# Performance work log

Measured on AMD Instinct MI355X. Metric: run time of the kernel, lower is better.

## Reference

```python
import jax, jax.numpy as jnp
import numpy as np

N, E, B = 50000, 800000, 1000
NODE_DIN, BB_DOUT, DHID, K = 32, 64, 64, 3
GLOB_DIN, EMBED_DIN = 64, 64
CIN = BB_DOUT + NODE_DIN  # 96


def setup_inputs() -> dict:
    key = jax.random.key(0)
    ks = jax.random.split(key, 24)

    def w(k, shape, fan_in):
        return jax.random.normal(k, shape, jnp.float32) / np.float32(np.sqrt(fan_in))

    inp = dict(
        x=jax.random.normal(ks[0], (N, NODE_DIN), jnp.float32),
        u=jax.random.normal(ks[1], (B, GLOB_DIN), jnp.float32),
        z=jax.random.normal(ks[2], (N, BB_DOUT), jnp.float32),
        edge_index=jax.random.randint(ks[3], (2, E), 0, N),
        edge_weight=jax.random.uniform(ks[4], (E,), jnp.float32),
        batch=jnp.sort(jax.random.randint(ks[5], (N,), 0, B)),
        batch_size=B,
        prev_h=jax.random.normal(ks[6], (N, DHID), jnp.float32),
    )
    # six ChebConvs of GConvGRU: x-convs take CIN, h-convs take DHID; all output DHID
    for i, nm in enumerate(["xz", "hz", "xr", "hr", "xh", "hh"]):
        cin = CIN if nm[0] == "x" else DHID
        inp[f"W{nm}"] = w(ks[7 + 2 * i], (K, cin, DHID), cin * K)
        inp[f"b{nm}"] = jnp.zeros((DHID,), jnp.float32)
    inp["Wg"] = w(ks[20], (GLOB_DIN, EMBED_DIN), GLOB_DIN)
    inp["bg"] = jnp.zeros((EMBED_DIN,), jnp.float32)
    return inp


def _cheb(xin, W, b, src, dst, w_norm, n):
    """ChebConv with sym norm, lambda_max=2 -> L_hat = -D^-1/2 A D^-1/2 (diag cancels)."""
    def prop(t):  # L_hat @ t  ([N,C])
        return -jax.ops.segment_sum(w_norm[:, None] * t[src], dst, num_segments=n)

    out = xin @ W[0] + b
    tx_prev = xin
    tx = None
    if W.shape[0] > 1:
        tx = prop(xin)
        out = out + tx @ W[1]
    for k in range(2, W.shape[0]):
        tx_new = 2.0 * prop(tx) - tx_prev
        out = out + tx_new @ W[k]
        tx_prev, tx = tx, tx_new
    return out


def reference(x, u, z, edge_index, edge_weight, batch, batch_size, prev_h,
              Wxz, bxz, Whz, bhz, Wxr, bxr, Whr, bhr, Wxh, bxh, Whh, bhh, Wg, bg):
    n = x.shape[0]
    src, dst = edge_index[0], edge_index[1]
    deg = jax.ops.segment_sum(edge_weight, src, num_segments=n)
    deg_safe = jnp.where(deg > 0, deg, 1.0)
    dinv = jnp.where(deg > 0, jax.lax.rsqrt(deg_safe), 0.0)
    w_norm = dinv[src] * edge_weight * dinv[dst]

    xin = jnp.concatenate([z, x], axis=-1)  # [N, CIN]
    Z = jax.nn.sigmoid(_cheb(xin, Wxz, bxz, src, dst, w_norm, n)
                       + _cheb(prev_h, Whz, bhz, src, dst, w_norm, n))
    R = jax.nn.sigmoid(_cheb(xin, Wxr, bxr, src, dst, w_norm, n)
                       + _cheb(prev_h, Whr, bhr, src, dst, w_norm, n))
    Ht = jnp.tanh(_cheb(xin, Wxh, bxh, src, dst, w_norm, n)
                  + _cheb(prev_h * R, Whh, bhh, src, dst, w_norm, n))
    h = Z * prev_h + (1.0 - Z) * Ht

    graph_emb = jax.ops.segment_sum(z, batch, num_segments=batch_size)  # [B, BB_DOUT]
    global_emb = jax.nn.relu(u @ Wg + bg)                                # [B, EMBED_DIN]
    fused = jnp.concatenate([graph_emb, global_emb], axis=-1)           # [B, 128]
    return fused, h
```

## Files before the change

kernel.cpp:

```cpp
#include <hip/hip_runtime.h>

#define NN 50000
#define EE 800000
#define BB 1000
#define NB 196
#define NR 8
#define RS 6272
#define NC 32
#define CHUNK 25000

#define NRB 160
#define RSB 314
#define NBIN 256
#define CH2 3125
#define CAP 7000

typedef unsigned short u16;
typedef unsigned long long u64;
typedef __attribute__((ext_vector_type(8))) short bf16x8;
typedef __attribute__((ext_vector_type(4))) float f32x4;

static __device__ __forceinline__ u16 f2b(float f) {
    union { float f; unsigned u; } v;
    v.f = f;
    unsigned r = v.u + 0x7fffu + ((v.u >> 16) & 1u);
    return (u16)(r >> 16);
}

static __device__ __forceinline__ float b2f(short s) {
    union { unsigned u; float f; } c;
    c.u = ((unsigned)(u16)s) << 16;
    return c.f;
}

__global__ __launch_bounds__(512) void k_degcnt_lds(
    const int* __restrict__ src, const int* __restrict__ dst,
    const float* __restrict__ ew, float* __restrict__ deg_p,
    int* __restrict__ cnt_p) {
    __shared__ float sdeg[RS];
    __shared__ int scnt[RS];
    int r = blockIdx.x & (NR - 1);
    int c = blockIdx.x >> 3;
    int base = r * RS;
    for (int i = threadIdx.x; i < RS; i += 512) {
        sdeg[i] = 0.f;
        scnt[i] = 0;
    }
    __syncthreads();
    int e0 = c * CHUNK;
    for (int j = threadIdx.x; j < CHUNK; j += 512) {
        int e = e0 + j;
        int s = src[e], d = dst[e];
        int sl = s - base, dl = d - base;
        if ((unsigned)sl < RS) atomicAdd(&sdeg[sl], ew[e]);
        if ((unsigned)dl < RS) atomicAdd(&scnt[dl], 1);
    }
    __syncthreads();
    int lim = (NN - base < RS) ? (NN - base) : RS;
    for (int i = threadIdx.x; i < lim; i += 512) {
        deg_p[(size_t)c * NN + base + i] = sdeg[i];
        cnt_p[(size_t)c * NN + base + i] = scnt[i];
    }
}

__global__ void k_scan1(const int* __restrict__ cnt_p, int* __restrict__ cnt,
                        int* __restrict__ incl, int* __restrict__ bsum) {
    __shared__ int s[256];
    int i = blockIdx.x * 256 + threadIdx.x;
    int v = 0;
    if (i < NN) {
#pragma unroll
        for (int p = 0; p < NC; p++) v += cnt_p[(size_t)p * NN + i];
        cnt[i] = v;
    }
    s[threadIdx.x] = v;
    __syncthreads();
    for (int off = 1; off < 256; off <<= 1) {
        int t = (threadIdx.x >= off) ? s[threadIdx.x - off] : 0;
        __syncthreads();
        s[threadIdx.x] += t;
        __syncthreads();
    }
    if (i < NN) incl[i] = s[threadIdx.x];
    if (threadIdx.x == 255) bsum[blockIdx.x] = s[255];
}

__global__ void k_scan2(int* __restrict__ bsum) {
    __shared__ int s[256];
    int v = (threadIdx.x < NB) ? bsum[threadIdx.x] : 0;
    s[threadIdx.x] = v;
    __syncthreads();
    for (int off = 1; off < 256; off <<= 1) {
        int t = (threadIdx.x >= off) ? s[threadIdx.x - off] : 0;
        __syncthreads();
        s[threadIdx.x] += t;
        __syncthreads();
    }
    if (threadIdx.x < NB) bsum[threadIdx.x] = s[threadIdx.x];
}

__global__ void k_scan3(const int* __restrict__ incl, const int* __restrict__ cnt,
                        const int* __restrict__ bsum, int* __restrict__ row_ptr,
                        int* __restrict__ scur, const float* __restrict__ deg_p,
                        float* __restrict__ dinv) {
    int i = blockIdx.x * 256 + threadIdx.x;
    if (i >= NN) return;
    int off = (blockIdx.x > 0) ? bsum[blockIdx.x - 1] : 0;
    int start = off + incl[i] - cnt[i];
    row_ptr[i] = start;
    if (i % RSB == 0) scur[i / RSB] = start;
    float d = 0.f;
#pragma unroll
    for (int p = 0; p < NC; p++) d += deg_p[(size_t)p * NN + i];
    dinv[i] = d > 0.f ? rsqrtf(d) : 0.f;
}

__global__ __launch_bounds__(512) void k_bin(
    const int* __restrict__ src, const int* __restrict__ dst,
    const float* __restrict__ ew, const float* __restrict__ dinv,
    int* __restrict__ scur, u64* __restrict__ stage) {
    __shared__ int cntA[NRB], baseB[NRB], rk[NRB];
    int e0 = blockIdx.x * CH2;
    for (int i = threadIdx.x; i < NRB; i += 512) cntA[i] = 0;
    __syncthreads();
    for (int j = threadIdx.x; j < CH2; j += 512) {
        int d = dst[e0 + j];
        atomicAdd(&cntA[d / RSB], 1);
    }
    __syncthreads();
    for (int i = threadIdx.x; i < NRB; i += 512) {
        baseB[i] = atomicAdd(&scur[i], cntA[i]);
        rk[i] = 0;
    }
    __syncthreads();
    for (int j = threadIdx.x; j < CH2; j += 512) {
        int e = e0 + j;
        int d = dst[e], s = src[e];
        int r = d / RSB;
        int slot = baseB[r] + atomicAdd(&rk[r], 1);
        float w = dinv[s] * ew[e] * dinv[d];
        unsigned dl = (unsigned)(d - r * RSB);
        u64 rec = ((u64)((dl << 16) | (unsigned)s) << 32) | (u64)__float_as_uint(w);
        stage[slot] = rec;
    }
}

__global__ __launch_bounds__(512) void k_sortrange(
    const u64* __restrict__ stage, const int* __restrict__ row_ptr,
    uint2* __restrict__ csr8) {
    __shared__ uint2 img[CAP];
    __shared__ int cur[RSB];
    int r = blockIdx.x;
    int r0 = r * RSB;
    int nrows = (NN - r0 < RSB) ? (NN - r0) : RSB;
    int p0 = row_ptr[r0];
    int p1 = (r0 + nrows < NN) ? row_ptr[r0 + nrows] : EE;
    for (int i = threadIdx.x; i < nrows; i += 512) cur[i] = row_ptr[r0 + i] - p0;
    __syncthreads();
    int n = p1 - p0;
    for (int j = threadIdx.x; j < n; j += 512) {
        u64 rec = stage[p0 + j];
        unsigned hi = (unsigned)(rec >> 32);
        int pos = atomicAdd(&cur[hi >> 16], 1);
        img[pos] = make_uint2(hi & 0xffffu, (unsigned)(rec & 0xffffffffu));
    }
    __syncthreads();
    for (int j = threadIdx.x; j < n; j += 512) csr8[p0 + j] = img[j];
}

__global__ void k_build_A(const float* __restrict__ z, const float* __restrict__ x,
                          const float* __restrict__ ph, u16* __restrict__ A) {
    int i = blockIdx.x * 256 + threadIdx.x;
    if (i >= NN * 160) return;
    int n = i / 160, c = i - n * 160;
    float v;
    if (c < 64) v = z[n * 64 + c];
    else if (c < 96) v = x[n * 32 + (c - 64)];
    else v = ph[n * 64 + (c - 96)];
    A[(size_t)n * 480 + c] = f2b(v);
}

__global__ void k_packW_all(const float* __restrict__ Wxz, const float* __restrict__ Wxr,
                            const float* __restrict__ Wxh, const float* __restrict__ Whz,
                            const float* __restrict__ Whr, const float* __restrict__ Whh,
                            u16* __restrict__ Wp, u16* __restrict__ W3p) {
    int idx = blockIdx.x * 256 + threadIdx.x;
    if (idx < 15 * 12 * 512) {
        int j = idx & 7, l = (idx >> 3) & 63;
        int ct = (idx >> 9) % 12, s = (idx >> 9) / 12;
        int k = 32 * s + (l >> 4) * 8 + j;
        int g = ct >> 2;
        int c = 16 * (ct & 3) + (l & 15);
        bool isX;
        int kr;
        if (k < 96)       { isX = true;  kr = k; }
        else if (k < 160) { isX = false; kr = k - 96; }
        else if (k < 256) { isX = true;  kr = 96 + (k - 160); }
        else if (k < 320) { isX = false; kr = 64 + (k - 256); }
        else if (k < 416) { isX = true;  kr = 192 + (k - 320); }
        else              { isX = false; kr = 128 + (k - 416); }
        float val;
        if (isX) {
            const float* W = (g == 0) ? Wxz : ((g == 1) ? Wxr : Wxh);
            val = W[kr * 64 + c];
        } else if (g == 2) {
            val = 0.f;
        } else {
            const float* W = (g == 0) ? Whz : Whr;
            val = W[kr * 64 + c];
        }
        Wp[idx] = f2b(val);
    } else {
        int i2 = idx - 15 * 12 * 512;
        if (i2 >= 6 * 4 * 512) return;
        int j = i2 & 7, l = (i2 >> 3) & 63;
        int ct = (i2 >> 9) & 3, s = i2 >> 11;
        int k = 32 * s + (l >> 4) * 8 + j;
        int ki = k >> 6, kr = k & 63;
        int c = 16 * ct + (l & 15);
        W3p[i2] = f2b(Whh[(ki * 64 + kr) * 64 + c]);
    }
}

template <int C, int SCALE, bool HB, int BS, int OS>
__global__ __launch_bounds__(BS) void k_pull(
    const u16* __restrict__ Abase, int inofs, int baseofs, int outofs,
    const uint2* __restrict__ csr8, const int* __restrict__ row_ptr,
    const int* __restrict__ cnt) {
    constexpr int TPR = C / 8;
    int tid = blockIdx.x * BS + threadIdx.x;
    int r = tid / TPR;
    int c8 = (tid - r * TPR) * 8;
    if (r >= NN) return;
    int s0 = row_ptr[r], n = cnt[r];
    float acc[8] = {0.f, 0.f, 0.f, 0.f, 0.f, 0.f, 0.f, 0.f};
    const u16* in = Abase + inofs + c8;
    uint2 e = (n > 0) ? csr8[s0] : make_uint2(0u, 0u);
    for (int j = 0; j < n; j++) {
        uint2 ec = e;
        if (j + 1 < n) e = csr8[s0 + j + 1];
        float w = __uint_as_float(ec.y);
        bf16x8 v = *(const bf16x8*)(in + (size_t)ec.x * OS);
#pragma unroll
        for (int k = 0; k < 8; k++) acc[k] += w * b2f(v[k]);
    }
    const float sc = -(float)SCALE;
    float o[8];
    if (HB) {
        bf16x8 b = *(const bf16x8*)(Abase + (size_t)r * OS + baseofs + c8);
#pragma unroll
        for (int k = 0; k < 8; k++) o[k] = sc * acc[k] - b2f(b[k]);
    } else {
#pragma unroll
        for (int k = 0; k < 8; k++) o[k] = sc * acc[k];
    }
    bf16x8 p;
#pragma unroll
    for (int k = 0; k < 8; k++) p[k] = (short)f2b(o[k]);
    *(bf16x8*)(const_cast<u16*>(Abase) + (size_t)r * OS + outofs + c8) = p;
}

__global__ __launch_bounds__(256) void k_gates_mfma(
    const u16* __restrict__ A, const u16* __restrict__ Wp,
    const float* __restrict__ bxz, const float* __restrict__ bhz,
    const float* __restrict__ bxr, const float* __restrict__ bhr,
    const float* __restrict__ bxh,
    u16* __restrict__ Zb16, u16* __restrict__ Hx16, u16* __restrict__ A3) {
    int gw = (blockIdx.x * 256 + threadIdx.x) >> 6;
    int tile = gw / 3;
    int g = gw - tile * 3;
    int r0 = tile * 16;
    if (r0 >= NN) return;
    int lane = threadIdx.x & 63;
    int q = lane >> 4, j0 = lane & 15;

    f32x4 acc[4];
#pragma unroll
    for (int i = 0; i < 4; i++) acc[i] = (f32x4){0.f, 0.f, 0.f, 0.f};

    const u16* arow = A + (size_t)(r0 + j0) * 480 + q * 8;
    if (g < 2) {
        const u16* bp0 = Wp + (size_t)(g * 4) * 512 + lane * 8;
#pragma unroll
        for (int s = 0; s < 15; s++) {
            bf16x8 a = *(const bf16x8*)(arow + 32 * s);
            const u16* bp = bp0 + (size_t)(s * 12) * 512;
#pragma unroll
            for (int ct = 0; ct < 4; ct++) {
                bf16x8 b = *(const bf16x8*)(bp + ct * 512);
                acc[ct] = __builtin_amdgcn_mfma_f32_16x16x32_bf16(a, b, acc[ct], 0, 0, 0);
            }
        }
    } else {
        const int slist[9] = {0, 1, 2, 5, 6, 7, 10, 11, 12};
        const u16* bp0 = Wp + (size_t)8 * 512 + lane * 8;
#pragma unroll
        for (int si = 0; si < 9; si++) {
            int s = slist[si];
            bf16x8 a = *(const bf16x8*)(arow + 32 * s);
            const u16* bp = bp0 + (size_t)(s * 12) * 512;
#pragma unroll
            for (int ct = 0; ct < 4; ct++) {
                bf16x8 b = *(const bf16x8*)(bp + ct * 512);
                acc[ct] = __builtin_amdgcn_mfma_f32_16x16x32_bf16(a, b, acc[ct], 0, 0, 0);
            }
        }
    }

    if (g == 0) {
#pragma unroll
        for (int ct = 0; ct < 4; ct++) {
            int j = 16 * ct + j0;
            float bz = bxz[j] + bhz[j];
#pragma unroll
            for (int reg = 0; reg < 4; reg++) {
                int r = r0 + q * 4 + reg;
                float zv = 1.f / (1.f + expf(-(acc[ct][reg] + bz)));
                Zb16[(size_t)r * 64 + j] = f2b(zv);
            }
        }
    } else if (g == 1) {
#pragma unroll
        for (int ct = 0; ct < 4; ct++) {
            int j = 16 * ct + j0;
            float br = bxr[j] + bhr[j];
#pragma unroll
            for (int reg = 0; reg < 4; reg++) {
                int r = r0 + q * 4 + reg;
                float rv = 1.f / (1.f + expf(-(acc[ct][reg] + br)));
                float phv = b2f((short)A[(size_t)r * 480 + 96 + j]);
                A3[(size_t)r * 192 + j] = f2b(rv * phv);
            }
        }
    } else {
#pragma unroll
        for (int ct = 0; ct < 4; ct++) {
            int j = 16 * ct + j0;
            float bh = bxh[j];
#pragma unroll
            for (int reg = 0; reg < 4; reg++) {
                int r = r0 + q * 4 + reg;
                Hx16[(size_t)r * 64 + j] = f2b(acc[ct][reg] + bh);
            }
        }
    }
}

__global__ __launch_bounds__(256) void k_final_mfma(
    const u16* __restrict__ A3, const u16* __restrict__ W3p,
    const float* __restrict__ bhh, const u16* __restrict__ Hx16,
    const u16* __restrict__ Zb16, const u16* __restrict__ A,
    float* __restrict__ outh) {
    int wv = (blockIdx.x * 256 + threadIdx.x) >> 6;
    int lane = threadIdx.x & 63;
    int r0 = wv * 16;
    if (r0 >= NN) return;
    int q = lane >> 4, j0 = lane & 15;

    f32x4 acc[4];
#pragma unroll
    for (int i = 0; i < 4; i++) acc[i] = (f32x4){0.f, 0.f, 0.f, 0.f};

    const u16* arow = A3 + (size_t)(r0 + j0) * 192 + q * 8;
#pragma unroll
    for (int s = 0; s < 6; s++) {
        bf16x8 a = *(const bf16x8*)(arow + 32 * s);
        const u16* bp = W3p + (size_t)(s * 4) * 512 + lane * 8;
#pragma unroll
        for (int ct = 0; ct < 4; ct++) {
            bf16x8 b = *(const bf16x8*)(bp + ct * 512);
            acc[ct] = __builtin_amdgcn_mfma_f32_16x16x32_bf16(a, b, acc[ct], 0, 0, 0);
        }
    }

#pragma unroll
    for (int ct = 0; ct < 4; ct++) {
        int j = 16 * ct + j0;
        float bh = bhh[j];
#pragma unroll
        for (int reg = 0; reg < 4; reg++) {
            int r = r0 + q * 4 + reg;
            size_t i = (size_t)r * 64 + j;
            float ht = tanhf(b2f((short)Hx16[i]) + acc[ct][reg] + bh);
            float zv = b2f((short)Zb16[i]);
            float phv = b2f((short)A[(size_t)r * 480 + 96 + j]);
            outh[i] = zv * phv + (1.f - zv) * ht;
        }
    }
}

__global__ __launch_bounds__(256) void k_tail(
    const float* __restrict__ z, const int* __restrict__ batch,
    const float* __restrict__ u, const float* __restrict__ Wg,
    const float* __restrict__ bg, float* __restrict__ out) {
    int b = (blockIdx.x * 256 + threadIdx.x) >> 6;
    int lane = threadIdx.x & 63;
    if (b >= BB) return;
    int lo = 0, hi = NN;
    while (lo < hi) {
        int m = (lo + hi) >> 1;
        if (batch[m] < b) lo = m + 1; else hi = m;
    }
    int start = lo;
    hi = NN;
    while (lo < hi) {
        int m = (lo + hi) >> 1;
        if (batch[m] < b + 1) lo = m + 1; else hi = m;
    }
    int end = lo;
    float acc = 0.f;
    for (int n = start; n < end; n++) acc += z[(size_t)n * 64 + lane];
    float g = bg[lane];
    const float* ur = u + (size_t)b * 64;
    for (int k = 0; k < 64; k++) g += ur[k] * Wg[k * 64 + lane];
    g = fmaxf(g, 0.f);
    out[(size_t)b * 128 + lane] = acc;
    out[(size_t)b * 128 + 64 + lane] = g;
}

extern "C" void kernel_launch(void* const* d_in, const int* in_sizes, int n_in,
                              void* d_out, int out_size, void* d_ws, size_t ws_size,
                              hipStream_t stream) {
    const float* x  = (const float*)d_in[0];
    const float* u  = (const float*)d_in[1];
    const float* z  = (const float*)d_in[2];
    const int*   ei = (const int*)d_in[3];
    const float* ew = (const float*)d_in[4];
    const int* batch = (const int*)d_in[5];
    const float* ph = (const float*)d_in[7];
    const float *Wxz = (const float*)d_in[8],  *bxz = (const float*)d_in[9];
    const float *Whz = (const float*)d_in[10], *bhz = (const float*)d_in[11];
    const float *Wxr = (const float*)d_in[12], *bxr = (const float*)d_in[13];
    const float *Whr = (const float*)d_in[14], *bhr = (const float*)d_in[15];
    const float *Wxh = (const float*)d_in[16], *bxh = (const float*)d_in[17];
    const float *Whh = (const float*)d_in[18], *bhh = (const float*)d_in[19];
    const float *Wg  = (const float*)d_in[20], *bg  = (const float*)d_in[21];
    const int* src = ei;
    const int* dst = ei + EE;

    char* wsb = (char*)d_ws;
    size_t o = 0;
    auto alloc = [&](size_t bytes) {
        void* p = wsb + o;
        o += (bytes + 255) & ~(size_t)255;
        return p;
    };
    float* deg_p   = (float*)alloc((size_t)NC * NN * 4);
    int*   cnt_p   = (int*)alloc((size_t)NC * NN * 4);
    int*   cnt     = (int*)alloc(NN * 4);
    int*   incl    = (int*)alloc(NN * 4);
    int*   row_ptr = (int*)alloc(NN * 4);
    float* dinv    = (float*)alloc(NN * 4);
    int*   bsum    = (int*)alloc(256 * 4);
    int*   scur    = (int*)alloc(NRB * 4);
    uint2* csr8    = (uint2*)alloc((size_t)EE * 8);
    u16*   Zb16 = (u16*)alloc((size_t)NN * 64 * 2);
    u16*   Hx16 = (u16*)alloc((size_t)NN * 64 * 2);
    u16*   A    = (u16*)alloc((size_t)NN * 480 * 2);
    u16*   A3   = (u16*)alloc((size_t)NN * 192 * 2);
    u16*   Wp   = (u16*)alloc(15 * 12 * 512 * 2);
    u16*   W3p  = (u16*)alloc(6 * 4 * 512 * 2);
    u64*   stage = (u64*)deg_p;

    float* outF = (float*)d_out;
    float* outH = outF + (size_t)BB * 128;

    const int BLK = 256;
    const int gA = (NN * 160 + BLK - 1) / BLK;
    const int gPull160 = (NN + 15) / 16;
    const int gPull64 = (NN + 31) / 32;
    const int gGates = (3 * 3125 + 3) / 4;
    const int gMFMA = (3125 + 3) / 4;
    const int gPack = (15 * 12 * 512 + 6 * 4 * 512 + BLK - 1) / BLK;

    k_packW_all<<<gPack, BLK, 0, stream>>>(Wxz, Wxr, Wxh, Whz, Whr, Whh, Wp, W3p);
    k_build_A<<<gA, BLK, 0, stream>>>(z, x, ph, A);

    k_degcnt_lds<<<NR * NC, 512, 0, stream>>>(src, dst, ew, deg_p, cnt_p);

    k_scan1<<<NB, 256, 0, stream>>>(cnt_p, cnt, incl, bsum);
    k_scan2<<<1, 256, 0, stream>>>(bsum);
    k_scan3<<<NB, 256, 0, stream>>>(incl, cnt, bsum, row_ptr, scur, deg_p, dinv);

    k_bin<<<NBIN, 512, 0, stream>>>(src, dst, ew, dinv, scur, stage);
    k_sortrange<<<NRB, 512, 0, stream>>>(stage, row_ptr, csr8);

    k_pull<160, 1, false, 320, 480><<<gPull160, 320, 0, stream>>>(A, 0, 0, 160, csr8, row_ptr, cnt);
    k_pull<160, 2, true, 320, 480><<<gPull160, 320, 0, stream>>>(A, 160, 0, 320, csr8, row_ptr, cnt);

    k_gates_mfma<<<gGates, BLK, 0, stream>>>(A, Wp, bxz, bhz, bxr, bhr, bxh, Zb16, Hx16, A3);

    k_pull<64, 1, false, 256, 192><<<gPull64, 256, 0, stream>>>(A3, 0, 0, 64, csr8, row_ptr, cnt);
    k_pull<64, 2, true, 256, 192><<<gPull64, 256, 0, stream>>>(A3, 64, 0, 128, csr8, row_ptr, cnt);

    k_final_mfma<<<gMFMA, BLK, 0, stream>>>(A3, W3p, bhh, Hx16, Zb16, A, outH);

    k_tail<<<(BB * 64 + BLK - 1) / BLK, BLK, 0, stream>>>(z, batch, u, Wg, bg, outF);
}
```

Baseline: 418.6 us.

## Split sparse pull features into column-chunk planes for cache-friendly gathers

Gather sources for the Chebyshev propagation are now stored in separate column-chunk arrays (8 chunks of 20 or 8 bf16 channels each), and each pull block handles one chunk. The goal is a smaller working set per block, so random neighbor gathers hit in cache instead of striding through the wide 480- or 192-element rows. The cost is extra writes, since every result goes to both the row-major A buffer and a chunked copy, plus more kernel blocks that each reread the CSR edges per chunk. Some of the chunked buffers reuse scratch memory from the degree and count stages.

```diff
diff --git a/kernel.cpp b/kernel.cpp
--- a/kernel.cpp
+++ b/kernel.cpp
@@ -18,6 +18,7 @@
 typedef unsigned short u16;
 typedef unsigned long long u64;
 typedef __attribute__((ext_vector_type(8))) short bf16x8;
+typedef __attribute__((ext_vector_type(4))) short bf16x4;
 typedef __attribute__((ext_vector_type(4))) float f32x4;
 
 static __device__ __forceinline__ u16 f2b(float f) {
@@ -169,7 +170,8 @@
 }
 
 __global__ void k_build_A(const float* __restrict__ z, const float* __restrict__ x,
-                          const float* __restrict__ ph, u16* __restrict__ A) {
+                          const float* __restrict__ ph, u16* __restrict__ A,
+                          u16* __restrict__ G0) {
     int i = blockIdx.x * 256 + threadIdx.x;
     if (i >= NN * 160) return;
     int n = i / 160, c = i - n * 160;
@@ -177,7 +179,10 @@
     if (c < 64) v = z[n * 64 + c];
     else if (c < 96) v = x[n * 32 + (c - 64)];
     else v = ph[n * 64 + (c - 96)];
-    A[(size_t)n * 480 + c] = f2b(v);
+    u16 v16 = f2b(v);
+    A[(size_t)n * 480 + c] = v16;
+    int ck = c / 20, cl = c - ck * 20;
+    G0[((size_t)ck * NN + n) * 20 + cl] = v16;
 }
 
 __global__ void k_packW_all(const float* __restrict__ Wxz, const float* __restrict__ Wxr,
@@ -222,42 +227,71 @@
     }
 }
 
-template <int C, int SCALE, bool HB, int BS, int OS>
-__global__ __launch_bounds__(BS) void k_pull(
-    const u16* __restrict__ Abase, int inofs, int baseofs, int outofs,
+template <int CPC, int TPR, int SCALE, bool HB, int OS, int BS>
+__global__ __launch_bounds__(BS) void k_pull_c(
+    const u16* __restrict__ Gin, const u16* __restrict__ Gbase,
+    u16* __restrict__ Gout, u16* __restrict__ Arow, int outofs,
     const uint2* __restrict__ csr8, const int* __restrict__ row_ptr,
     const int* __restrict__ cnt) {
-    constexpr int TPR = C / 8;
-    int tid = blockIdx.x * BS + threadIdx.x;
-    int r = tid / TPR;
-    int c8 = (tid - r * TPR) * 8;
+    constexpr int CW = CPC / TPR;
+    constexpr int RPB = BS / TPR;
+    int c = blockIdx.x & 7;
+    int team = threadIdx.x / TPR;
+    int t = threadIdx.x - team * TPR;
+    int r = (blockIdx.x >> 3) * RPB + team;
     if (r >= NN) return;
+    const u16* gin = Gin + ((size_t)c * NN) * CPC + t * CW;
     int s0 = row_ptr[r], n = cnt[r];
-    float acc[8] = {0.f, 0.f, 0.f, 0.f, 0.f, 0.f, 0.f, 0.f};
-    const u16* in = Abase + inofs + c8;
+    float acc[CW];
+#pragma unroll
+    for (int k = 0; k < CW; k++) acc[k] = 0.f;
     uint2 e = (n > 0) ? csr8[s0] : make_uint2(0u, 0u);
     for (int j = 0; j < n; j++) {
         uint2 ec = e;
         if (j + 1 < n) e = csr8[s0 + j + 1];
         float w = __uint_as_float(ec.y);
-        bf16x8 v = *(const bf16x8*)(in + (size_t)ec.x * OS);
-#pragma unroll
-        for (int k = 0; k < 8; k++) acc[k] += w * b2f(v[k]);
+        const u16* sp = gin + (size_t)ec.x * CPC;
+        if constexpr (CW == 8) {
+            bf16x8 v = *(const bf16x8*)sp;
+#pragma unroll
+            for (int k = 0; k < 8; k++) acc[k] += w * b2f(v[k]);
+        } else {
+            bf16x4 v = *(const bf16x4*)sp;
+#pragma unroll
+            for (int k = 0; k < 4; k++) acc[k] += w * b2f(v[k]);
+        }
     }
     const float sc = -(float)SCALE;
-    float o[8];
+    float o[CW];
     if (HB) {
-        bf16x8 b = *(const bf16x8*)(Abase + (size_t)r * OS + baseofs + c8);
-#pragma unroll
-        for (int k = 0; k < 8; k++) o[k] = sc * acc[k] - b2f(b[k]);
+        const u16* bp = Gbase + ((size_t)c * NN + r) * CPC + t * CW;
+        if constexpr (CW == 8) {
+            bf16x8 b = *(const bf16x8*)bp;
+#pragma unroll
+            for (int k = 0; k < 8; k++) o[k] = sc * acc[k] - b2f(b[k]);
+        } else {
+            bf16x4 b = *(const bf16x4*)bp;
+#pragma unroll
+            for (int k = 0; k < 4; k++) o[k] = sc * acc[k] - b2f(b[k]);
+        }
     } else {
 #pragma unroll
-        for (int k = 0; k < 8; k++) o[k] = sc * acc[k];
-    }
-    bf16x8 p;
-#pragma unroll
-    for (int k = 0; k < 8; k++) p[k] = (short)f2b(o[k]);
-    *(bf16x8*)(const_cast<u16*>(Abase) + (size_t)r * OS + outofs + c8) = p;
+        for (int k = 0; k < CW; k++) o[k] = sc * acc[k];
+    }
+    u16* arow = Arow + (size_t)r * OS + outofs + c * CPC + t * CW;
+    if constexpr (CW == 8) {
+        bf16x8 p;
+#pragma unroll
+        for (int k = 0; k < 8; k++) p[k] = (short)f2b(o[k]);
+        *(bf16x8*)arow = p;
+        if (Gout) *(bf16x8*)(Gout + ((size_t)c * NN + r) * CPC + t * CW) = p;
+    } else {
+        bf16x4 p;
+#pragma unroll
+        for (int k = 0; k < 4; k++) p[k] = (short)f2b(o[k]);
+        *(bf16x4*)arow = p;
+        if (Gout) *(bf16x4*)(Gout + ((size_t)c * NN + r) * CPC + t * CW) = p;
+    }
 }
 
 __global__ __launch_bounds__(256) void k_gates_mfma(
@@ -265,7 +299,8 @@
     const float* __restrict__ bxz, const float* __restrict__ bhz,
     const float* __restrict__ bxr, const float* __restrict__ bhr,
     const float* __restrict__ bxh,
-    u16* __restrict__ Zb16, u16* __restrict__ Hx16, u16* __restrict__ A3) {
+    u16* __restrict__ Zb16, u16* __restrict__ Hx16, u16* __restrict__ A3,
+    u16* __restrict__ G3) {
     int gw = (blockIdx.x * 256 + threadIdx.x) >> 6;
     int tile = gw / 3;
     int g = gw - tile * 3;
@@ -329,7 +364,9 @@
                 int r = r0 + q * 4 + reg;
                 float rv = 1.f / (1.f + expf(-(acc[ct][reg] + br)));
                 float phv = b2f((short)A[(size_t)r * 480 + 96 + j]);
-                A3[(size_t)r * 192 + j] = f2b(rv * phv);
+                u16 pv = f2b(rv * phv);
+                A3[(size_t)r * 192 + j] = pv;
+                G3[((size_t)(j >> 3) * NN + r) * 8 + (j & 7)] = pv;
             }
         }
     } else {
@@ -460,21 +497,25 @@
     u16*   A3   = (u16*)alloc((size_t)NN * 192 * 2);
     u16*   Wp   = (u16*)alloc(15 * 12 * 512 * 2);
     u16*   W3p  = (u16*)alloc(6 * 4 * 512 * 2);
+    u16*   G0   = (u16*)alloc((size_t)NN * 160 * 2);
+    u16*   G1   = (u16*)alloc((size_t)NN * 160 * 2);
     u64*   stage = (u64*)deg_p;
+    u16*   G3    = (u16*)deg_p;
+    u16*   G4    = (u16*)cnt_p;
 
     float* outF = (float*)d_out;
     float* outH = outF + (size_t)BB * 128;
 
     const int BLK = 256;
     const int gA = (NN * 160 + BLK - 1) / BLK;
-    const int gPull160 = (NN + 15) / 16;
-    const int gPull64 = (NN + 31) / 32;
+    const int gPc160 = 8 * ((NN + 63) / 64);
+    const int gPc64  = 8 * ((NN + 255) / 256);
     const int gGates = (3 * 3125 + 3) / 4;
     const int gMFMA = (3125 + 3) / 4;
     const int gPack = (15 * 12 * 512 + 6 * 4 * 512 + BLK - 1) / BLK;
 
     k_packW_all<<<gPack, BLK, 0, stream>>>(Wxz, Wxr, Wxh, Whz, Whr, Whh, Wp, W3p);
-    k_build_A<<<gA, BLK, 0, stream>>>(z, x, ph, A);
+    k_build_A<<<gA, BLK, 0, stream>>>(z, x, ph, A, G0);
 
     k_degcnt_lds<<<NR * NC, 512, 0, stream>>>(src, dst, ew, deg_p, cnt_p);
 
@@ -485,13 +526,18 @@
     k_bin<<<NBIN, 512, 0, stream>>>(src, dst, ew, dinv, scur, stage);
     k_sortrange<<<NRB, 512, 0, stream>>>(stage, row_ptr, csr8);
 
-    k_pull<160, 1, false, 320, 480><<<gPull160, 320, 0, stream>>>(A, 0, 0, 160, csr8, row_ptr, cnt);
-    k_pull<160, 2, true, 320, 480><<<gPull160, 320, 0, stream>>>(A, 160, 0, 320, csr8, row_ptr, cnt);
-
-    k_gates_mfma<<<gGates, BLK, 0, stream>>>(A, Wp, bxz, bhz, bxr, bhr, bxh, Zb16, Hx16, A3);
-
-    k_pull<64, 1, false, 256, 192><<<gPull64, 256, 0, stream>>>(A3, 0, 0, 64, csr8, row_ptr, cnt);
-    k_pull<64, 2, true, 256, 192><<<gPull64, 256, 0, stream>>>(A3, 64, 0, 128, csr8, row_ptr, cnt);
+    k_pull_c<20, 5, 1, false, 480, 320><<<gPc160, 320, 0, stream>>>(
+        G0, nullptr, G1, A, 160, csr8, row_ptr, cnt);
+    k_pull_c<20, 5, 2, true, 480, 320><<<gPc160, 320, 0, stream>>>(
+        G1, G0, nullptr, A, 320, csr8, row_ptr, cnt);
+
+    k_gates_mfma<<<gGates, BLK, 0, stream>>>(A, Wp, bxz, bhz, bxr, bhr, bxh,
+                                             Zb16, Hx16, A3, G3);
+
+    k_pull_c<8, 1, 1, false, 192, 256><<<gPc64, 256, 0, stream>>>(
+        G3, nullptr, G4, A3, 64, csr8, row_ptr, cnt);
+    k_pull_c<8, 1, 2, true, 192, 256><<<gPc64, 256, 0, stream>>>(
+        G4, G3, nullptr, A3, 128, csr8, row_ptr, cnt);
 
     k_final_mfma<<<gMFMA, BLK, 0, stream>>>(A3, W3p, bhh, Hx16, Zb16, A, outH);
 
```

Result: slower. 597.0 us (+42.6%).
